# Kernel optimization log

Hardware: AMD Instinct MI355X
Metric: run time of the kernel (lower is better)

The kernel has to match this reference:

```python
import jax, jax.numpy as jnp
import numpy as np


def setup_inputs() -> dict:
    key = jax.random.key(0)
    k1, k2 = jax.random.split(key)
    B, N, D = 32, 1024, 384
    x = jax.random.normal(k1, (B, N, D), dtype=jnp.float32)
    durations = jax.random.randint(k2, (B, N), 0, 8, dtype=jnp.int32)
    return {"x": x, "durations": durations, "max_len": 4096}


def reference(x, durations, max_len):
    # x: (B, N, D) encoder output; durations: (B, N) frames per phoneme.
    # Fused length-regulation: for each output frame t, source phoneme index is
    # the smallest n with cumsum(durations)[n] > t (searchsorted right on cumsum).
    B, N, D = x.shape
    cum = jnp.cumsum(durations, axis=1)              # (B, N)
    total = cum[:, -1]                               # (B,) total frames per row
    t = jnp.arange(max_len, dtype=cum.dtype)         # (T,)
    # (B, T) source index per output frame
    idx = jax.vmap(lambda c: jnp.searchsorted(c, t, side="right"))(cum)
    mel_mask = t[None, :] >= total[:, None]          # (B, T) True where padding
    idx_c = jnp.minimum(idx, N - 1)                  # clamp out-of-range (padded frames)
    out = jnp.take_along_axis(x, idx_c[:, :, None], axis=1)   # (B, T, D)
    out = jnp.where(mel_mask[:, :, None], jnp.zeros((), x.dtype), out)
    return out, mel_mask
```

## Files before the change

kernel.cpp:

```cpp
#include <hip/hip_runtime.h>

#define BB 32
#define NN 1024
#define DD 384
#define ML 4096
#define D4 (DD / 4)
#define TOTF4 (BB * ML * D4)
#define CT 256
#define NBLK (TOTF4 / CT)

__global__ __launch_bounds__(CT) void lr_scan_kernel(
    const int4* __restrict__ dur4, int* __restrict__ idxb,
    float* __restrict__ mask) {
    __shared__ __align__(16) int idx_lds[ML];
    __shared__ int wsum[CT / 64];
    const int b    = blockIdx.x;
    const int tid  = threadIdx.x;
    const int lane = tid & 63;
    const int wid  = tid >> 6;

    int4 d = dur4[b * (NN / 4) + tid];
    int4* lds4 = reinterpret_cast<int4*>(idx_lds);
    #pragma unroll
    for (int k = 0; k < ML / 4 / CT; ++k)
        lds4[tid + k * CT] = make_int4(-1, -1, -1, -1);

    int s = d.x + d.y + d.z + d.w;
    #pragma unroll
    for (int off = 1; off < 64; off <<= 1) {
        int n = __shfl_up(s, off);
        if (lane >= off) s += n;
    }
    if (lane == 63) wsum[wid] = s;
    __syncthreads();
    int woff = 0;
    #pragma unroll
    for (int w = 0; w < CT / 64 - 1; ++w)
        if (w < wid) woff += wsum[w];

    int c3 = woff + s;
    int c2 = c3 - d.w;
    int c1 = c2 - d.z;
    int c0 = c1 - d.y;
    int p  = c0 - d.x;

    const int i0 = tid * 4;
    int lo, hi;
    lo = p;  hi = (c0 < ML) ? c0 : ML; for (int t = lo; t < hi; ++t) idx_lds[t] = i0;
    lo = c0; hi = (c1 < ML) ? c1 : ML; for (int t = lo; t < hi; ++t) idx_lds[t] = i0 + 1;
    lo = c1; hi = (c2 < ML) ? c2 : ML; for (int t = lo; t < hi; ++t) idx_lds[t] = i0 + 2;
    lo = c2; hi = (c3 < ML) ? c3 : ML; for (int t = lo; t < hi; ++t) idx_lds[t] = i0 + 3;
    __syncthreads();

    int4* idxb4 = reinterpret_cast<int4*>(idxb + b * ML);
    float4* mask4 = reinterpret_cast<float4*>(mask + b * ML);
    #pragma unroll
    for (int k = 0; k < ML / 4 / CT; ++k) {
        const int4 v = lds4[tid + k * CT];
        idxb4[tid + k * CT] = v;
        float4 m;
        m.x = (v.x < 0) ? 1.0f : 0.0f;
        m.y = (v.y < 0) ? 1.0f : 0.0f;
        m.z = (v.z < 0) ? 1.0f : 0.0f;
        m.w = (v.w < 0) ? 1.0f : 0.0f;
        mask4[tid + k * CT] = m;
    }
}

__global__ __launch_bounds__(CT) void lr_flat_copy_kernel(
    const float4* __restrict__ x, const int* __restrict__ idxb,
    float4* __restrict__ out) {
    const int g   = ((blockIdx.x & 7) * (NBLK / 8)) + (blockIdx.x >> 3);
    const int gid = g * CT + threadIdx.x;
    const int row = gid / D4;
    const int d4  = gid - row * D4;
    const int idx = idxb[row];
    float4 v = {0.0f, 0.0f, 0.0f, 0.0f};
    if (idx >= 0) {
        const int b = row >> 12;
        v = x[((b << 10) + idx) * D4 + d4];
    }
    out[gid] = v;
}

extern "C" void kernel_launch(void* const* d_in, const int* in_sizes, int n_in,
                              void* d_out, int out_size, void* d_ws, size_t ws_size,
                              hipStream_t stream) {
    const float* x = (const float*)d_in[0];
    const int* dur = (const int*)d_in[1];

    int* idxb   = (int*)d_ws;
    float* out  = (float*)d_out;
    float* mask = out + (size_t)BB * ML * DD;

    lr_scan_kernel<<<BB, CT, 0, stream>>>((const int4*)dur, idxb, mask);
    lr_flat_copy_kernel<<<NBLK, CT, 0, stream>>>(
        (const float4*)x, idxb, (float4*)out);
}
```

Baseline: 251.3 us.

## Use persistent multi-item copy blocks with batched loads and nontemporal stores

The copy kernel changes from one float4 per thread across many blocks to 2048 blocks where each thread handles many float4s. Index loads and gathers are issued in groups of eight to raise memory-level parallelism. Output writes use nontemporal stores to avoid polluting cache. In exchange there are fewer blocks in flight and more register pressure from the unrolled groups.

```diff
diff --git a/kernel.cpp b/kernel.cpp
--- a/kernel.cpp
+++ b/kernel.cpp
@@ -7,7 +7,13 @@
 #define D4 (DD / 4)
 #define TOTF4 (BB * ML * D4)
 #define CT 256
-#define NBLK (TOTF4 / CT)
+#define CB 2048
+#define F4B (TOTF4 / CB)
+#define KIT (F4B / CT)
+#define GRP 8
+#define NGRP (KIT / GRP)
+
+typedef float f32x4 __attribute__((ext_vector_type(4)));
 
 __global__ __launch_bounds__(CT) void lr_scan_kernel(
     const int4* __restrict__ dur4, int* __restrict__ idxb,
@@ -67,20 +73,39 @@
     }
 }
 
-__global__ __launch_bounds__(CT) void lr_flat_copy_kernel(
+__global__ __launch_bounds__(CT) void lr_copy_kernel(
     const float4* __restrict__ x, const int* __restrict__ idxb,
     float4* __restrict__ out) {
-    const int g   = ((blockIdx.x & 7) * (NBLK / 8)) + (blockIdx.x >> 3);
-    const int gid = g * CT + threadIdx.x;
-    const int row = gid / D4;
-    const int d4  = gid - row * D4;
-    const int idx = idxb[row];
-    float4 v = {0.0f, 0.0f, 0.0f, 0.0f};
-    if (idx >= 0) {
-        const int b = row >> 12;
-        v = x[((b << 10) + idx) * D4 + d4];
+    const int g    = ((blockIdx.x & 7) * (CB / 8)) + (blockIdx.x >> 3);
+    const int base = g * F4B + threadIdx.x;
+
+    #pragma unroll
+    for (int grp = 0; grp < NGRP; ++grp) {
+        int    idxv[GRP];
+        float4 v[GRP];
+        #pragma unroll
+        for (int j = 0; j < GRP; ++j) {
+            const int gid = base + (grp * GRP + j) * CT;
+            const int row = gid / D4;
+            idxv[j] = idxb[row];
+        }
+        #pragma unroll
+        for (int j = 0; j < GRP; ++j) {
+            const int gid = base + (grp * GRP + j) * CT;
+            const int row = gid / D4;
+            const int d4  = gid - row * D4;
+            const int b   = row >> 12;
+            v[j] = make_float4(0.0f, 0.0f, 0.0f, 0.0f);
+            if (idxv[j] >= 0)
+                v[j] = x[((b << 10) + idxv[j]) * D4 + d4];
+        }
+        #pragma unroll
+        for (int j = 0; j < GRP; ++j) {
+            const int gid = base + (grp * GRP + j) * CT;
+            f32x4* dst = reinterpret_cast<f32x4*>(&out[gid]);
+            __builtin_nontemporal_store(*reinterpret_cast<f32x4*>(&v[j]), dst);
+        }
     }
-    out[gid] = v;
 }
 
 extern "C" void kernel_launch(void* const* d_in, const int* in_sizes, int n_in,
@@ -94,6 +119,6 @@
     float* mask = out + (size_t)BB * ML * DD;
 
     lr_scan_kernel<<<BB, CT, 0, stream>>>((const int4*)dur, idxb, mask);
-    lr_flat_copy_kernel<<<NBLK, CT, 0, stream>>>(
+    lr_copy_kernel<<<CB, CT, 0, stream>>>(
         (const float4*)x, idxb, (float4*)out);
 }
```

After: 249.4 us. About the same (-0.8%).
